# Performance work log

Measured on AMD Instinct MI355X. Metric: run time of the kernel, lower is better.

Reference implementation:

```python
import jax, jax.numpy as jnp
import numpy as np

# ---- static configuration (matches init_kwargs) ----
B = 256              # graph pairs -> 2B graphs total (query/corpus interleaved)
N_PER_GRAPH = 24     # nodes per graph
N_MAX = 32           # max node set size (transport plan side)
E_PER_GRAPH = 200    # edges per graph
E_MAX = 256          # max_edge_set_size
D_EDGE = 256         # edge_feature_dim
D_SINK = 256         # sinkhorn_feature_dim
TEMPERATURE = 0.1
NUM_SINKHORN_ITERS = 20
NOISE_FACTOR = 0.0   # deterministic sinkhorn
CONSISTENCY_WEIGHT = 1.0


def setup_inputs() -> dict:
    rng = np.random.RandomState(0)
    num_graphs = 2 * B
    node_offset = np.arange(num_graphs) * N_PER_GRAPH
    graph_idx = np.repeat(np.arange(num_graphs), N_PER_GRAPH)
    # edges are grouped by graph (standard batched-graph layout)
    from_local = rng.randint(0, N_PER_GRAPH, size=(num_graphs, E_PER_GRAPH))
    to_local = rng.randint(0, N_PER_GRAPH, size=(num_graphs, E_PER_GRAPH))
    from_idx = (from_local + node_offset[:, None]).reshape(-1)
    to_idx = (to_local + node_offset[:, None]).reshape(-1)
    total_edges = num_graphs * E_PER_GRAPH

    key = jax.random.key(0)
    k = jax.random.split(key, 4)
    return {
        "edge_features_enc": jax.random.normal(k[0], (total_edges, D_EDGE), jnp.float32),
        "node_transport_plan": jax.random.uniform(k[1], (B, N_MAX, N_MAX), jnp.float32),
        "W1": jax.random.normal(k[2], (D_EDGE, D_SINK), jnp.float32) / np.sqrt(D_EDGE).astype(np.float32),
        "b1": jnp.zeros((D_SINK,), jnp.float32),
        "W2": jax.random.normal(k[3], (D_SINK, D_SINK), jnp.float32) / np.sqrt(D_SINK).astype(np.float32),
        "b2": jnp.zeros((D_SINK,), jnp.float32),
        "from_idx": jnp.asarray(from_idx, jnp.int32),
        "to_idx": jnp.asarray(to_idx, jnp.int32),
        "graph_idx": jnp.asarray(graph_idx, jnp.int32),
        "query_sizes": jnp.full((B,), N_PER_GRAPH, jnp.int32),
        "corpus_sizes": jnp.full((B,), N_PER_GRAPH, jnp.int32),
    }


def reference(edge_features_enc, node_transport_plan, W1, b1, W2, b2,
              from_idx, to_idx, graph_idx, query_sizes, corpus_sizes):
    num_graphs = 2 * B
    total_edges = from_idx.shape[0]

    # --- get_paired_edge_counts / split_and_stack ---
    g_edge = graph_idx[from_idx]                                   # graph id per edge
    edge_counts = jax.ops.segment_sum(jnp.ones_like(g_edge), g_edge, num_segments=num_graphs)
    edge_offset = jnp.cumsum(edge_counts) - edge_counts            # exclusive prefix
    rank = jnp.arange(total_edges, dtype=jnp.int32) - edge_offset[g_edge]

    stacked = jnp.zeros((num_graphs, E_MAX, D_EDGE), edge_features_enc.dtype)
    stacked = stacked.at[g_edge, rank].set(edge_features_enc)      # [2B, E_MAX, D]
    q_feat, c_feat = stacked[0::2], stacked[1::2]

    # --- sinkhorn_feature_layers (Linear-ReLU-Linear) + size mask ---
    def mlp(x):
        return jax.nn.relu(x @ W1 + b1) @ W2 + b2
    q_feat, c_feat = mlp(q_feat), mlp(c_feat)
    pos = jnp.arange(E_MAX)
    q_feat = q_feat * (pos[None, :] < query_sizes[:, None]).astype(q_feat.dtype)[..., None]
    c_feat = c_feat * (pos[None, :] < corpus_sizes[:, None]).astype(c_feat.dtype)[..., None]

    # --- kronecker_product_on_nodes: local endpoint ids, pad slots -> zero row N_MAX ---
    node_counts = jax.ops.segment_sum(jnp.ones_like(graph_idx), graph_idx, num_segments=num_graphs)
    node_offset = jnp.cumsum(node_counts) - node_counts
    pad = jnp.full((num_graphs, E_MAX), N_MAX, jnp.int32)
    f_loc = pad.at[g_edge, rank].set(from_idx - node_offset[g_edge])
    t_loc = pad.at[g_edge, rank].set(to_idx - node_offset[g_edge])
    fq, fc = f_loc[0::2], f_loc[1::2]
    tq, tc = t_loc[0::2], t_loc[1::2]

    T = jnp.pad(node_transport_plan, ((0, 0), (0, 1), (0, 1)))     # zero row/col for pads
    b = jnp.arange(B)[:, None, None]
    straight = T[b, fq[:, :, None], fc[:, None, :]] * T[b, tq[:, :, None], tc[:, None, :]]
    cross = T[b, fq[:, :, None], tc[:, None, :]] * T[b, tq[:, :, None], fc[:, None, :]]

    # --- sinkhorn_iters (log domain, noise_factor=0) ---
    log_alpha = (straight + cross) / TEMPERATURE                   # [B, E_MAX, E_MAX]
    def step(la, _):
        la = la - jax.nn.logsumexp(la, axis=2, keepdims=True)
        la = la - jax.nn.logsumexp(la, axis=1, keepdims=True)
        return la, None
    log_alpha, _ = jax.lax.scan(step, log_alpha, None, length=NUM_SINKHORN_ITERS)
    plan = jnp.exp(log_alpha)

    # --- feature_alignment_score: -sum(relu(q - P c)) per pair ---
    score = -jax.nn.relu(q_feat - plan @ c_feat).sum(axis=(1, 2))
    return CONSISTENCY_WEIGHT * score
```

## Files before the change

kernel.cpp:

```cpp
#include <hip/hip_runtime.h>

typedef unsigned short ushort_t;
typedef unsigned int uint_t;

typedef float f32x4_t __attribute__((ext_vector_type(4)));
typedef short s16x8_t __attribute__((ext_vector_type(8)));

#define NB   256
#define NG   512
#define NPG  24
#define NMAXI 32
#define EPG  200
#define DD   256
#define L2E_OVER_T 14.426950408889634f

__device__ __forceinline__ ushort_t f2bf(float f) {
    uint_t u = __float_as_uint(f);
    u += 0x7FFFu + ((u >> 16) & 1u);
    return (ushort_t)(u >> 16);
}
__device__ __forceinline__ float bfhi(uint_t u) { return __uint_as_float(u & 0xFFFF0000u); }
__device__ __forceinline__ float bflo(uint_t u) { return __uint_as_float(u << 16); }

__device__ __forceinline__ float frcp(float x) {
#if __has_builtin(__builtin_amdgcn_rcpf)
    return __builtin_amdgcn_rcpf(x);
#else
    return 1.0f / x;
#endif
}

template <int CTRL>
__device__ __forceinline__ float dpp_radd(float s) {
    int d = __builtin_amdgcn_update_dpp(0, __float_as_int(s), CTRL, 0xF, 0xF, true);
    return s + __int_as_float(d);
}
__device__ __forceinline__ float row16_reduce_dpp(float s) {
    s = dpp_radd<0xB1>(s);
    s = dpp_radd<0x4E>(s);
    s = dpp_radd<0x141>(s);
    s = dpp_radd<0x140>(s);
    return s;
}

__global__ __launch_bounds__(256) void prep_w(const float* __restrict__ W1,
                                              const float* __restrict__ W2,
                                              ushort_t* __restrict__ W1T,
                                              ushort_t* __restrict__ W2T)
{
    __shared__ float tile[2][4 * 256];
    const int t = threadIdx.x;
    const int k0 = blockIdx.x * 4;
    #pragma unroll
    for (int i = t; i < 4 * 256; i += 256) {
        tile[0][i] = W1[k0 * 256 + i];
        tile[1][i] = W2[k0 * 256 + i];
    }
    __syncthreads();
    const int n = t;
    #pragma unroll
    for (int m = 0; m < 2; ++m) {
        uint_t p0 = (uint_t)f2bf(tile[m][0 * 256 + n]) | ((uint_t)f2bf(tile[m][1 * 256 + n]) << 16);
        uint_t p1 = (uint_t)f2bf(tile[m][2 * 256 + n]) | ((uint_t)f2bf(tile[m][3 * 256 + n]) << 16);
        ushort_t* dst = (m ? W2T : W1T) + n * 256 + k0;
        uint2 pk; pk.x = p0; pk.y = p1;
        *(uint2*)dst = pk;
    }
}

__global__ __launch_bounds__(256) void mlp_kernel(
    const float* __restrict__ X, const ushort_t* __restrict__ W1T,
    const ushort_t* __restrict__ W2T, const float* __restrict__ b1,
    const float* __restrict__ b2, float* __restrict__ Y)
{
    __shared__ ushort_t sA[16 * 272];
    const int t = threadIdx.x;
    const int blk = blockIdx.x;
    const int lane = t & 63;
    const int w = t >> 6;
    const int quad = lane >> 4;
    const int mrow = lane & 15;

    {
        int r = t >> 4;
        int ch = (t & 15) * 16;
        int rho = blk * 16 + r;
        int g = rho / NPG;
        int e = rho - g * NPG;
        const float* src = X + ((size_t)(g * EPG + e)) * DD + ch;
        ushort_t* dst = &sA[r * 272 + ch];
        #pragma unroll
        for (int i = 0; i < 2; ++i) {
            float4 v0 = *(const float4*)(src + i * 8);
            float4 v1 = *(const float4*)(src + i * 8 + 4);
            uint4 pk;
            pk.x = (uint_t)f2bf(v0.x) | ((uint_t)f2bf(v0.y) << 16);
            pk.y = (uint_t)f2bf(v0.z) | ((uint_t)f2bf(v0.w) << 16);
            pk.z = (uint_t)f2bf(v1.x) | ((uint_t)f2bf(v1.y) << 16);
            pk.w = (uint_t)f2bf(v1.z) | ((uint_t)f2bf(v1.w) << 16);
            *(uint4*)(dst + i * 8) = pk;
        }
    }
    __syncthreads();

    f32x4_t acc[4];
    #pragma unroll
    for (int i = 0; i < 4; ++i) acc[i] = (f32x4_t){0.f, 0.f, 0.f, 0.f};

    #pragma unroll
    for (int k0 = 0; k0 < 256; k0 += 32) {
        s16x8_t a = *(const s16x8_t*)&sA[mrow * 272 + k0 + quad * 8];
        #pragma unroll
        for (int nt = 0; nt < 4; ++nt) {
            s16x8_t bb = *(const s16x8_t*)(W1T + (size_t)(64 * w + nt * 16 + mrow) * 256 + k0 + quad * 8);
            acc[nt] = __builtin_amdgcn_mfma_f32_16x16x32_bf16(a, bb, acc[nt], 0, 0, 0);
        }
    }
    __syncthreads();

    #pragma unroll
    for (int nt = 0; nt < 4; ++nt) {
        int col = 64 * w + nt * 16 + mrow;
        float bias = b1[col];
        f32x4_t v = acc[nt];
        #pragma unroll
        for (int reg = 0; reg < 4; ++reg) {
            int row = quad * 4 + reg;
            sA[row * 272 + col] = f2bf(fmaxf(v[reg] + bias, 0.f));
        }
    }
    __syncthreads();

    #pragma unroll
    for (int i = 0; i < 4; ++i) acc[i] = (f32x4_t){0.f, 0.f, 0.f, 0.f};

    #pragma unroll
    for (int k0 = 0; k0 < 256; k0 += 32) {
        s16x8_t a = *(const s16x8_t*)&sA[mrow * 272 + k0 + quad * 8];
        #pragma unroll
        for (int nt = 0; nt < 4; ++nt) {
            s16x8_t bb = *(const s16x8_t*)(W2T + (size_t)(64 * w + nt * 16 + mrow) * 256 + k0 + quad * 8);
            acc[nt] = __builtin_amdgcn_mfma_f32_16x16x32_bf16(a, bb, acc[nt], 0, 0, 0);
        }
    }

    #pragma unroll
    for (int nt = 0; nt < 4; ++nt) {
        int col = 64 * w + nt * 16 + mrow;
        float bias = b2[col];
        f32x4_t v = acc[nt];
        #pragma unroll
        for (int reg = 0; reg < 4; ++reg) {
            int row = blk * 16 + quad * 4 + reg;
            Y[(size_t)row * 256 + col] = v[reg] + bias;
        }
    }
}

__global__ __launch_bounds__(1024) void sink_kernel(
    const float* __restrict__ Tplan, const int* __restrict__ from_idx,
    const int* __restrict__ to_idx, const int* __restrict__ qsz,
    const int* __restrict__ csz, const float* __restrict__ qcf,
    float* __restrict__ out)
{
    const int b = blockIdx.x;
    const int t = threadIdx.x;
    const int R = t >> 4;
    const int C = t & 15;
    const int w = t >> 6;

    __shared__ __align__(16) char ovl[56320];
    __shared__ float ru_s[260];
    __shared__ float rv_p[320];
    __shared__ float wsum[16];

    float* Tl = (float*)ovl;
    int* fq = (int*)(ovl + 4368);
    int* tq = (int*)(ovl + 5392);
    int* fc = (int*)(ovl + 6416);
    int* tc = (int*)(ovl + 7440);
    float* Vp = (float*)ovl;
    float* plan_s = (float*)ovl;
    float* cf_s   = (float*)(ovl + 25600);

    for (int i = t; i < 33 * 33; i += 1024) Tl[i] = 0.f;
    if (t < 320) rv_p[t] = 1.0f;
    if (t < 256) {
        int gq = 2 * b, gc = 2 * b + 1;
        int a = NMAXI, bb = NMAXI, c = NMAXI, d = NMAXI;
        if (t < EPG) {
            a  = from_idx[gq * EPG + t] - gq * NPG;
            bb = to_idx  [gq * EPG + t] - gq * NPG;
            c  = from_idx[gc * EPG + t] - gc * NPG;
            d  = to_idx  [gc * EPG + t] - gc * NPG;
        }
        fq[t] = a; tq[t] = bb; fc[t] = c; tc[t] = d;
    }
    __syncthreads();
    {
        int i = t >> 5, j = t & 31;
        Tl[i * 33 + j] = Tplan[((size_t)b << 10) + t];
    }
    __syncthreads();

    uint_t Kp[4][8];
    {
        int fcl[16], tcl[16];
        #pragma unroll
        for (int o = 0; o < 16; ++o) { fcl[o] = fc[16 * C + o]; tcl[o] = tc[16 * C + o]; }
        #pragma unroll
        for (int i = 0; i < 4; ++i) {
            const float* T1 = &Tl[fq[4 * R + i] * 33];
            const float* T2 = &Tl[tq[4 * R + i] * 33];
            #pragma unroll
            for (int u = 0; u < 8; ++u) {
                int f0 = fcl[2 * u], t0 = tcl[2 * u];
                int f1 = fcl[2 * u + 1], t1 = tcl[2 * u + 1];
                float la0 = T1[f0] * T2[t0] + T1[t0] * T2[f0];
                float la1 = T1[f1] * T2[t1] + T1[t1] * T2[f1];
                Kp[i][u] = (uint_t)f2bf(exp2f(la0 * L2E_OVER_T))
                         | ((uint_t)f2bf(exp2f(la1 * L2E_OVER_T)) << 16);
            }
        }
    }

    for (int it = 0; it < 20; ++it) {
        float uu[4];
        {
            float4 rv0 = *(const float4*)&rv_p[20 * C + 0];
            float4 rv1 = *(const float4*)&rv_p[20 * C + 4];
            float4 rv2 = *(const float4*)&rv_p[20 * C + 8];
            float4 rv3 = *(const float4*)&rv_p[20 * C + 12];
            #pragma unroll
            for (int i = 0; i < 4; ++i) {
                float a0 = bflo(Kp[i][0]) * rv0.x + bfhi(Kp[i][0]) * rv0.y;
                float a1 = bflo(Kp[i][1]) * rv0.z + bfhi(Kp[i][1]) * rv0.w;
                float a2 = bflo(Kp[i][2]) * rv1.x + bfhi(Kp[i][2]) * rv1.y;
                float a3 = bflo(Kp[i][3]) * rv1.z + bfhi(Kp[i][3]) * rv1.w;
                a0 += bflo(Kp[i][4]) * rv2.x + bfhi(Kp[i][4]) * rv2.y;
                a1 += bflo(Kp[i][5]) * rv2.z + bfhi(Kp[i][5]) * rv2.w;
                a2 += bflo(Kp[i][6]) * rv3.x + bfhi(Kp[i][6]) * rv3.y;
                a3 += bflo(Kp[i][7]) * rv3.z + bfhi(Kp[i][7]) * rv3.w;
                float s = (a0 + a1) + (a2 + a3);
                s = row16_reduce_dpp(s);
                uu[i] = frcp(s);
            }
            if (C == 0) {
                #pragma unroll
                for (int i = 0; i < 4; ++i) ru_s[4 * R + i] = uu[i];
            }
        }
        {
            #pragma unroll
            for (int h = 0; h < 2; ++h) {
                float pc[8];
                #pragma unroll
                for (int u = 0; u < 4; ++u) {
                    int uu_i = 4 * h + u;
                    float e0 = bflo(Kp[0][uu_i]) * uu[0] + bflo(Kp[1][uu_i]) * uu[1]
                             + bflo(Kp[2][uu_i]) * uu[2] + bflo(Kp[3][uu_i]) * uu[3];
                    float e1 = bfhi(Kp[0][uu_i]) * uu[0] + bfhi(Kp[1][uu_i]) * uu[1]
                             + bfhi(Kp[2][uu_i]) * uu[2] + bfhi(Kp[3][uu_i]) * uu[3];
                    pc[2 * u] = e0; pc[2 * u + 1] = e1;
                }
                #pragma unroll
                for (int k = 0; k < 8; ++k) {
                    float s = pc[k];
                    s += __shfl_xor(s, 16);
                    s += __shfl_xor(s, 32);
                    pc[k] = s;
                }
                if ((t & 63) < 16) {
                    float* dst = &Vp[w * 272 + C * 16 + 8 * h];
                    *(float4*)(dst + 0) = (float4){pc[0], pc[1], pc[2], pc[3]};
                    *(float4*)(dst + 4) = (float4){pc[4], pc[5], pc[6], pc[7]};
                }
            }
        }
        __syncthreads();
        if (t < 256) {
            float s = 0.f;
            #pragma unroll
            for (int ww = 0; ww < 16; ++ww) s += Vp[ww * 272 + t];
            rv_p[(t >> 4) * 20 + (t & 15)] = frcp(s);
        }
        __syncthreads();
    }

    int nq = qsz[b]; if (nq > 24) nq = 24;
    int nc = csz[b]; if (nc > 24) nc = 24;

    if (C < 2) {
        int umax = (C == 0) ? 8 : 4;
        #pragma unroll
        for (int i = 0; i < 4; ++i) {
            float rr = ru_s[4 * R + i];
            for (int u = 0; u < umax; ++u) {
                int j = 16 * C + 2 * u;
                plan_s[(4 * R + i) * 25 + j]     = bflo(Kp[i][u]) * rr * rv_p[20 * C + 2 * u];
                plan_s[(4 * R + i) * 25 + j + 1] = bfhi(Kp[i][u]) * rr * rv_p[20 * C + 2 * u + 1];
            }
        }
    }
    if (t < 768) {
        int j = t >> 5, inner = t & 31;
        int c = inner * 8;
        const float* src = qcf + ((size_t)(2 * b + 1) * 24 + j) * 256 + c;
        float4 v0 = *(const float4*)(src);
        float4 v1 = *(const float4*)(src + 4);
        float* dst = cf_s + j * 320 + (c >> 4) * 20 + (c & 15);
        *(float4*)dst = v0;
        *(float4*)(dst + 4) = v1;
    }
    __syncthreads();

    const int r0 = R * 4;
    const int m  = C;
    const float* qbase = qcf + (size_t)(2 * b) * 24 * 256;

    float ssum = 0.f;
    #pragma unroll
    for (int p = 0; p < 2; ++p) {
        float ps[32];
        #pragma unroll
        for (int i = 0; i < 32; ++i) ps[i] = 0.f;

        for (int j = 0; j < nc; ++j) {
            float p0 = plan_s[(r0 + 0) * 25 + j];
            float p1 = plan_s[(r0 + 1) * 25 + j];
            float p2 = plan_s[(r0 + 2) * 25 + j];
            float p3 = plan_s[(r0 + 3) * 25 + j];
            const float4* cfp = (const float4*)(cf_s + j * 320 + m * 20) + 2 * p;
            #pragma unroll
            for (int k = 0; k < 2; ++k) {
                float4 cv = cfp[k];
                ps[ 0 + k * 4 + 0] += p0 * cv.x; ps[ 0 + k * 4 + 1] += p0 * cv.y;
                ps[ 0 + k * 4 + 2] += p0 * cv.z; ps[ 0 + k * 4 + 3] += p0 * cv.w;
                ps[ 8 + k * 4 + 0] += p1 * cv.x; ps[ 8 + k * 4 + 1] += p1 * cv.y;
                ps[ 8 + k * 4 + 2] += p1 * cv.z; ps[ 8 + k * 4 + 3] += p1 * cv.w;
                ps[16 + k * 4 + 0] += p2 * cv.x; ps[16 + k * 4 + 1] += p2 * cv.y;
                ps[16 + k * 4 + 2] += p2 * cv.z; ps[16 + k * 4 + 3] += p2 * cv.w;
                ps[24 + k * 4 + 0] += p3 * cv.x; ps[24 + k * 4 + 1] += p3 * cv.y;
                ps[24 + k * 4 + 2] += p3 * cv.z; ps[24 + k * 4 + 3] += p3 * cv.w;
            }
        }

        #pragma unroll
        for (int i = 0; i < 4; ++i) {
            int row = r0 + i;
            if (row < nq) {
                const float4* qp = (const float4*)(qbase + (size_t)row * 256 + m * 16) + 2 * p;
                #pragma unroll
                for (int k = 0; k < 2; ++k) {
                    float4 qv = qp[k];
                    ssum += fmaxf(qv.x - ps[i * 8 + k * 4 + 0], 0.f);
                    ssum += fmaxf(qv.y - ps[i * 8 + k * 4 + 1], 0.f);
                    ssum += fmaxf(qv.z - ps[i * 8 + k * 4 + 2], 0.f);
                    ssum += fmaxf(qv.w - ps[i * 8 + k * 4 + 3], 0.f);
                }
            } else {
                #pragma unroll
                for (int k = 0; k < 8; ++k) ssum += fmaxf(-ps[i * 8 + k], 0.f);
            }
        }
    }

    ssum += __shfl_xor(ssum, 1);
    ssum += __shfl_xor(ssum, 2);
    ssum += __shfl_xor(ssum, 4);
    ssum += __shfl_xor(ssum, 8);
    ssum += __shfl_xor(ssum, 16);
    ssum += __shfl_xor(ssum, 32);
    if ((t & 63) == 0) wsum[t >> 6] = ssum;
    __syncthreads();
    if (t == 0) {
        float s = 0.f;
        #pragma unroll
        for (int i = 0; i < 16; ++i) s += wsum[i];
        out[b] = -s;
    }
}

extern "C" void kernel_launch(void* const* d_in, const int* in_sizes, int n_in,
                              void* d_out, int out_size, void* d_ws, size_t ws_size,
                              hipStream_t stream)
{
    const float* edge_feat = (const float*)d_in[0];
    const float* tplan     = (const float*)d_in[1];
    const float* W1        = (const float*)d_in[2];
    const float* b1        = (const float*)d_in[3];
    const float* W2        = (const float*)d_in[4];
    const float* b2        = (const float*)d_in[5];
    const int*   from_idx  = (const int*)d_in[6];
    const int*   to_idx    = (const int*)d_in[7];
    const int*   qsz       = (const int*)d_in[9];
    const int*   csz       = (const int*)d_in[10];
    float* out = (float*)d_out;

    char* ws = (char*)d_ws;
    ushort_t* W1T = (ushort_t*)ws;
    ushort_t* W2T = W1T + 65536;
    float* qcf = (float*)(ws + 262144);

    prep_w<<<64, 256, 0, stream>>>(W1, W2, W1T, W2T);
    mlp_kernel<<<768, 256, 0, stream>>>(edge_feat, W1T, W2T, b1, b2, qcf);
    sink_kernel<<<256, 1024, 0, stream>>>(tplan, from_idx, to_idx, qsz, csz, qcf, out);
}
```

Before: 263.1 us.

## Fuse edge-feature MLP into sinkhorn kernel, keeping features in LDS

The separate MLP kernel goes away. Each sinkhorn block now loads its own 48 edge rows (query and corpus), runs both bf16 MFMA GEMM layers in LDS, and keeps the resulting features in shared memory for the final alignment score. This removes one kernel launch and the global write and re-read of the projected features. In exchange the sinkhorn kernel needs about twice the shared memory and uses only 12 of its 16 waves during the MLP phase, which may lower occupancy and serialise the GEMM before the sinkhorn work.

```diff
diff --git a/kernel.cpp b/kernel.cpp
--- a/kernel.cpp
+++ b/kernel.cpp
@@ -68,99 +68,12 @@
     }
 }
 
-__global__ __launch_bounds__(256) void mlp_kernel(
-    const float* __restrict__ X, const ushort_t* __restrict__ W1T,
-    const ushort_t* __restrict__ W2T, const float* __restrict__ b1,
-    const float* __restrict__ b2, float* __restrict__ Y)
-{
-    __shared__ ushort_t sA[16 * 272];
-    const int t = threadIdx.x;
-    const int blk = blockIdx.x;
-    const int lane = t & 63;
-    const int w = t >> 6;
-    const int quad = lane >> 4;
-    const int mrow = lane & 15;
-
-    {
-        int r = t >> 4;
-        int ch = (t & 15) * 16;
-        int rho = blk * 16 + r;
-        int g = rho / NPG;
-        int e = rho - g * NPG;
-        const float* src = X + ((size_t)(g * EPG + e)) * DD + ch;
-        ushort_t* dst = &sA[r * 272 + ch];
-        #pragma unroll
-        for (int i = 0; i < 2; ++i) {
-            float4 v0 = *(const float4*)(src + i * 8);
-            float4 v1 = *(const float4*)(src + i * 8 + 4);
-            uint4 pk;
-            pk.x = (uint_t)f2bf(v0.x) | ((uint_t)f2bf(v0.y) << 16);
-            pk.y = (uint_t)f2bf(v0.z) | ((uint_t)f2bf(v0.w) << 16);
-            pk.z = (uint_t)f2bf(v1.x) | ((uint_t)f2bf(v1.y) << 16);
-            pk.w = (uint_t)f2bf(v1.z) | ((uint_t)f2bf(v1.w) << 16);
-            *(uint4*)(dst + i * 8) = pk;
-        }
-    }
-    __syncthreads();
-
-    f32x4_t acc[4];
-    #pragma unroll
-    for (int i = 0; i < 4; ++i) acc[i] = (f32x4_t){0.f, 0.f, 0.f, 0.f};
-
-    #pragma unroll
-    for (int k0 = 0; k0 < 256; k0 += 32) {
-        s16x8_t a = *(const s16x8_t*)&sA[mrow * 272 + k0 + quad * 8];
-        #pragma unroll
-        for (int nt = 0; nt < 4; ++nt) {
-            s16x8_t bb = *(const s16x8_t*)(W1T + (size_t)(64 * w + nt * 16 + mrow) * 256 + k0 + quad * 8);
-            acc[nt] = __builtin_amdgcn_mfma_f32_16x16x32_bf16(a, bb, acc[nt], 0, 0, 0);
-        }
-    }
-    __syncthreads();
-
-    #pragma unroll
-    for (int nt = 0; nt < 4; ++nt) {
-        int col = 64 * w + nt * 16 + mrow;
-        float bias = b1[col];
-        f32x4_t v = acc[nt];
-        #pragma unroll
-        for (int reg = 0; reg < 4; ++reg) {
-            int row = quad * 4 + reg;
-            sA[row * 272 + col] = f2bf(fmaxf(v[reg] + bias, 0.f));
-        }
-    }
-    __syncthreads();
-
-    #pragma unroll
-    for (int i = 0; i < 4; ++i) acc[i] = (f32x4_t){0.f, 0.f, 0.f, 0.f};
-
-    #pragma unroll
-    for (int k0 = 0; k0 < 256; k0 += 32) {
-        s16x8_t a = *(const s16x8_t*)&sA[mrow * 272 + k0 + quad * 8];
-        #pragma unroll
-        for (int nt = 0; nt < 4; ++nt) {
-            s16x8_t bb = *(const s16x8_t*)(W2T + (size_t)(64 * w + nt * 16 + mrow) * 256 + k0 + quad * 8);
-            acc[nt] = __builtin_amdgcn_mfma_f32_16x16x32_bf16(a, bb, acc[nt], 0, 0, 0);
-        }
-    }
-
-    #pragma unroll
-    for (int nt = 0; nt < 4; ++nt) {
-        int col = 64 * w + nt * 16 + mrow;
-        float bias = b2[col];
-        f32x4_t v = acc[nt];
-        #pragma unroll
-        for (int reg = 0; reg < 4; ++reg) {
-            int row = blk * 16 + quad * 4 + reg;
-            Y[(size_t)row * 256 + col] = v[reg] + bias;
-        }
-    }
-}
-
 __global__ __launch_bounds__(1024) void sink_kernel(
-    const float* __restrict__ Tplan, const int* __restrict__ from_idx,
-    const int* __restrict__ to_idx, const int* __restrict__ qsz,
-    const int* __restrict__ csz, const float* __restrict__ qcf,
+    const float* __restrict__ Tplan, const float* __restrict__ X,
+    const ushort_t* __restrict__ W1T, const ushort_t* __restrict__ W2T,
+    const float* __restrict__ b1, const float* __restrict__ b2,
+    const int* __restrict__ from_idx, const int* __restrict__ to_idx,
+    const int* __restrict__ qsz, const int* __restrict__ csz,
     float* __restrict__ out)
 {
     const int b = blockIdx.x;
@@ -168,22 +81,23 @@
     const int R = t >> 4;
     const int C = t & 15;
     const int w = t >> 6;
-
-    __shared__ __align__(16) char ovl[56320];
+    const int lane = t & 63;
+    const int quad = lane >> 4;
+    const int mrow = lane & 15;
+
+    __shared__ __align__(16) char ovl[113664];
+    __shared__ int fq_s[256], tq_s[256], fc_s[256], tc_s[256];
     __shared__ float ru_s[260];
     __shared__ float rv_p[320];
     __shared__ float wsum[16];
 
+    ushort_t* xa = (ushort_t*)ovl;
+    ushort_t* h1 = (ushort_t*)(ovl + 26112);
+    float*    qc = (float*)(ovl + 52224);
     float* Tl = (float*)ovl;
-    int* fq = (int*)(ovl + 4368);
-    int* tq = (int*)(ovl + 5392);
-    int* fc = (int*)(ovl + 6416);
-    int* tc = (int*)(ovl + 7440);
     float* Vp = (float*)ovl;
     float* plan_s = (float*)ovl;
-    float* cf_s   = (float*)(ovl + 25600);
-
-    for (int i = t; i < 33 * 33; i += 1024) Tl[i] = 0.f;
+
     if (t < 320) rv_p[t] = 1.0f;
     if (t < 256) {
         int gq = 2 * b, gc = 2 * b + 1;
@@ -194,8 +108,89 @@
             c  = from_idx[gc * EPG + t] - gc * NPG;
             d  = to_idx  [gc * EPG + t] - gc * NPG;
         }
-        fq[t] = a; tq[t] = bb; fc[t] = c; tc[t] = d;
-    }
+        fq_s[t] = a; tq_s[t] = bb; fc_s[t] = c; tc_s[t] = d;
+    }
+    {
+        int r = t >> 4;
+        if (r < 48) {
+            int half = (r >= 24);
+            int g = 2 * b + half;
+            int e = r - 24 * half;
+            int ch = (t & 15) * 16;
+            const float* src = X + ((size_t)(g * EPG + e)) * DD + ch;
+            ushort_t* dst = &xa[r * 272 + ch];
+            #pragma unroll
+            for (int i = 0; i < 2; ++i) {
+                float4 v0 = *(const float4*)(src + i * 8);
+                float4 v1 = *(const float4*)(src + i * 8 + 4);
+                uint4 pk;
+                pk.x = (uint_t)f2bf(v0.x) | ((uint_t)f2bf(v0.y) << 16);
+                pk.y = (uint_t)f2bf(v0.z) | ((uint_t)f2bf(v0.w) << 16);
+                pk.z = (uint_t)f2bf(v1.x) | ((uint_t)f2bf(v1.y) << 16);
+                pk.w = (uint_t)f2bf(v1.z) | ((uint_t)f2bf(v1.w) << 16);
+                *(uint4*)(dst + i * 8) = pk;
+            }
+        }
+    }
+    __syncthreads();
+
+    const int rc = w >> 2;
+    const int cc = w & 3;
+    if (rc < 3) {
+        f32x4_t acc[4];
+        #pragma unroll
+        for (int i = 0; i < 4; ++i) acc[i] = (f32x4_t){0.f, 0.f, 0.f, 0.f};
+        #pragma unroll
+        for (int k0 = 0; k0 < 256; k0 += 32) {
+            s16x8_t a = *(const s16x8_t*)&xa[(rc * 16 + mrow) * 272 + k0 + quad * 8];
+            #pragma unroll
+            for (int nt = 0; nt < 4; ++nt) {
+                s16x8_t bb = *(const s16x8_t*)(W1T + (size_t)(64 * cc + nt * 16 + mrow) * 256 + k0 + quad * 8);
+                acc[nt] = __builtin_amdgcn_mfma_f32_16x16x32_bf16(a, bb, acc[nt], 0, 0, 0);
+            }
+        }
+        #pragma unroll
+        for (int nt = 0; nt < 4; ++nt) {
+            int col = 64 * cc + nt * 16 + mrow;
+            float bias = b1[col];
+            f32x4_t v = acc[nt];
+            #pragma unroll
+            for (int reg = 0; reg < 4; ++reg) {
+                int row = rc * 16 + quad * 4 + reg;
+                h1[row * 272 + col] = f2bf(fmaxf(v[reg] + bias, 0.f));
+            }
+        }
+    }
+    __syncthreads();
+
+    if (rc < 3) {
+        f32x4_t acc[4];
+        #pragma unroll
+        for (int i = 0; i < 4; ++i) acc[i] = (f32x4_t){0.f, 0.f, 0.f, 0.f};
+        #pragma unroll
+        for (int k0 = 0; k0 < 256; k0 += 32) {
+            s16x8_t a = *(const s16x8_t*)&h1[(rc * 16 + mrow) * 272 + k0 + quad * 8];
+            #pragma unroll
+            for (int nt = 0; nt < 4; ++nt) {
+                s16x8_t bb = *(const s16x8_t*)(W2T + (size_t)(64 * cc + nt * 16 + mrow) * 256 + k0 + quad * 8);
+                acc[nt] = __builtin_amdgcn_mfma_f32_16x16x32_bf16(a, bb, acc[nt], 0, 0, 0);
+            }
+        }
+        #pragma unroll
+        for (int nt = 0; nt < 4; ++nt) {
+            int col = 64 * cc + nt * 16 + mrow;
+            float bias = b2[col];
+            f32x4_t v = acc[nt];
+            #pragma unroll
+            for (int reg = 0; reg < 4; ++reg) {
+                int row = rc * 16 + quad * 4 + reg;
+                qc[row * 320 + (4 * cc + nt) * 20 + mrow] = v[reg] + bias;
+            }
+        }
+    }
+    __syncthreads();
+
+    for (int i = t; i < 33 * 33; i += 1024) Tl[i] = 0.f;
     __syncthreads();
     {
         int i = t >> 5, j = t & 31;
@@ -207,11 +202,11 @@
     {
         int fcl[16], tcl[16];
         #pragma unroll
-        for (int o = 0; o < 16; ++o) { fcl[o] = fc[16 * C + o]; tcl[o] = tc[16 * C + o]; }
+        for (int o = 0; o < 16; ++o) { fcl[o] = fc_s[16 * C + o]; tcl[o] = tc_s[16 * C + o]; }
         #pragma unroll
         for (int i = 0; i < 4; ++i) {
-            const float* T1 = &Tl[fq[4 * R + i] * 33];
-            const float* T2 = &Tl[tq[4 * R + i] * 33];
+            const float* T1 = &Tl[fq_s[4 * R + i] * 33];
+            const float* T2 = &Tl[tq_s[4 * R + i] * 33];
             #pragma unroll
             for (int u = 0; u < 8; ++u) {
                 int f0 = fcl[2 * u], t0 = tcl[2 * u];
@@ -223,6 +218,7 @@
             }
         }
     }
+    __syncthreads();
 
     for (int it = 0; it < 20; ++it) {
         float uu[4];
@@ -256,11 +252,11 @@
                 float pc[8];
                 #pragma unroll
                 for (int u = 0; u < 4; ++u) {
-                    int uu_i = 4 * h + u;
-                    float e0 = bflo(Kp[0][uu_i]) * uu[0] + bflo(Kp[1][uu_i]) * uu[1]
-                             + bflo(Kp[2][uu_i]) * uu[2] + bflo(Kp[3][uu_i]) * uu[3];
-                    float e1 = bfhi(Kp[0][uu_i]) * uu[0] + bfhi(Kp[1][uu_i]) * uu[1]
-                             + bfhi(Kp[2][uu_i]) * uu[2] + bfhi(Kp[3][uu_i]) * uu[3];
+                    int ui = 4 * h + u;
+                    float e0 = bflo(Kp[0][ui]) * uu[0] + bflo(Kp[1][ui]) * uu[1]
+                             + bflo(Kp[2][ui]) * uu[2] + bflo(Kp[3][ui]) * uu[3];
+                    float e1 = bfhi(Kp[0][ui]) * uu[0] + bfhi(Kp[1][ui]) * uu[1]
+                             + bfhi(Kp[2][ui]) * uu[2] + bfhi(Kp[3][ui]) * uu[3];
                     pc[2 * u] = e0; pc[2 * u + 1] = e1;
                 }
                 #pragma unroll
@@ -302,21 +298,10 @@
             }
         }
     }
-    if (t < 768) {
-        int j = t >> 5, inner = t & 31;
-        int c = inner * 8;
-        const float* src = qcf + ((size_t)(2 * b + 1) * 24 + j) * 256 + c;
-        float4 v0 = *(const float4*)(src);
-        float4 v1 = *(const float4*)(src + 4);
-        float* dst = cf_s + j * 320 + (c >> 4) * 20 + (c & 15);
-        *(float4*)dst = v0;
-        *(float4*)(dst + 4) = v1;
-    }
     __syncthreads();
 
     const int r0 = R * 4;
     const int m  = C;
-    const float* qbase = qcf + (size_t)(2 * b) * 24 * 256;
 
     float ssum = 0.f;
     #pragma unroll
@@ -330,7 +315,7 @@
             float p1 = plan_s[(r0 + 1) * 25 + j];
             float p2 = plan_s[(r0 + 2) * 25 + j];
             float p3 = plan_s[(r0 + 3) * 25 + j];
-            const float4* cfp = (const float4*)(cf_s + j * 320 + m * 20) + 2 * p;
+            const float4* cfp = (const float4*)(qc + (24 + j) * 320 + m * 20) + 2 * p;
             #pragma unroll
             for (int k = 0; k < 2; ++k) {
                 float4 cv = cfp[k];
@@ -349,7 +334,7 @@
         for (int i = 0; i < 4; ++i) {
             int row = r0 + i;
             if (row < nq) {
-                const float4* qp = (const float4*)(qbase + (size_t)row * 256 + m * 16) + 2 * p;
+                const float4* qp = (const float4*)(qc + row * 320 + m * 20) + 2 * p;
                 #pragma unroll
                 for (int k = 0; k < 2; ++k) {
                     float4 qv = qp[k];
@@ -400,9 +385,8 @@
     char* ws = (char*)d_ws;
     ushort_t* W1T = (ushort_t*)ws;
     ushort_t* W2T = W1T + 65536;
-    float* qcf = (float*)(ws + 262144);
 
     prep_w<<<64, 256, 0, stream>>>(W1, W2, W1T, W2T);
-    mlp_kernel<<<768, 256, 0, stream>>>(edge_feat, W1T, W2T, b1, b2, qcf);
-    sink_kernel<<<256, 1024, 0, stream>>>(tplan, from_idx, to_idx, qsz, csz, qcf, out);
-}
+    sink_kernel<<<256, 1024, 0, stream>>>(tplan, edge_feat, W1T, W2T, b1, b2,
+                                          from_idx, to_idx, qsz, csz, out);
+}
```

After: 258.6 us. No clear change (-1.7%).
